# Optimization experiments

Hardware: AMD Instinct MI355X
Metric: run time of the kernel (lower is better)

The kernel has to match this reference:

```python
import jax, jax.numpy as jnp
import numpy as np


def setup_inputs() -> dict:
    key = jax.random.key(0)
    k1, k2, k3 = jax.random.split(key, 3)
    Q, M, D = 4096, 8192, 128
    query = jax.random.normal(k1, (Q, D), dtype=jnp.float32)
    memory_states = jax.random.normal(k2, (M, D), dtype=jnp.float32)
    weights = jax.random.uniform(k3, (Q, M), dtype=jnp.float32)
    return {"query": query, "memory_states": memory_states, "weights": weights}


def reference(query, memory_states, weights):
    d_k = query.shape[-1]
    # scores: [Q, M]
    scores = jnp.einsum('qd,md->qm', query, memory_states) / jnp.sqrt(jnp.asarray(d_k, query.dtype))
    attn = jax.nn.softmax(scores * weights, axis=-1)
    return jnp.einsum('qm,md->qd', attn, memory_states)
```

## Files before the change

kernel.cpp:

```cpp
#include <hip/hip_runtime.h>
#include <hip/hip_bf16.h>

typedef __attribute__((ext_vector_type(8))) short bf16x8;
typedef __attribute__((ext_vector_type(4))) float f32x4;

#define Qn 4096
#define Mn 8192
#define Dn 128
#define NWA 8
#define QB 128
#define MSPLIT 16
#define BCOLS (Mn / MSPLIT)
#define TILE 64
#define NIT (BCOLS / TILE)

__device__ __forceinline__ unsigned short f2bf(float x) {
  __hip_bfloat16 h = __float2bfloat16(x);
  return *reinterpret_cast<unsigned short*>(&h);
}

__device__ __forceinline__ void gld_lds16(const void* g, void* l) {
  __builtin_amdgcn_global_load_lds(
      (const __attribute__((address_space(1))) unsigned int*)g,
      (__attribute__((address_space(3))) unsigned int*)l, 16, 0, 0);
}

__global__ void zero_kernel(float4* __restrict__ p, int n4) {
  int i = blockIdx.x * blockDim.x + threadIdx.x;
  if (i < n4) p[i] = make_float4(0.f, 0.f, 0.f, 0.f);
}

__global__ void cast_q(const float4* __restrict__ Q4, ushort4* __restrict__ Qs) {
  int i = blockIdx.x * blockDim.x + threadIdx.x;
  const float s = 0.088388347648318447f;
  float4 q = Q4[i];
  Qs[i] = make_ushort4(f2bf(q.x * s), f2bf(q.y * s), f2bf(q.z * s), f2bf(q.w * s));
}

__global__ __launch_bounds__(256) void swz_kernel(const float* __restrict__ K,
                                                  unsigned short* __restrict__ Kswz,
                                                  unsigned short* __restrict__ Vswz) {
  __shared__ __align__(16) unsigned short T[64][72];
  const int m0 = blockIdx.x * 64, d0 = blockIdx.y * 64;
  const int t = threadIdx.x;
  const int r = t >> 4, c4 = (t & 15) * 4;
#pragma unroll
  for (int rr = 0; rr < 64; rr += 16) {
    float4 v = *reinterpret_cast<const float4*>(&K[(size_t)(m0 + r + rr) * Dn + d0 + c4]);
    ushort4 b = make_ushort4(f2bf(v.x), f2bf(v.y), f2bf(v.z), f2bf(v.w));
    *reinterpret_cast<ushort4*>(&T[r + rr][c4]) = b;
  }
  __syncthreads();
#pragma unroll
  for (int rep = 0; rep < 2; ++rep) {
    int w = t + rep * 256;
    int ml = w >> 3, oct = w & 7;
    uint4 val = *reinterpret_cast<uint4*>(&T[ml][oct * 8]);
    int m = m0 + ml, d = d0 + oct * 8;
    int g = m >> 4, l = m & 15, kk = d >> 5, quad = (d >> 3) & 3;
    *reinterpret_cast<uint4*>(&Kswz[(size_t)(((g * 4 + kk) * 64) + quad * 16 + l) * 8]) = val;
  }
#pragma unroll
  for (int rep = 0; rep < 2; ++rep) {
    int w = t + rep * 256;
    int dl = w >> 3, moct = w & 7;
    unsigned short tmp[8];
#pragma unroll
    for (int j = 0; j < 8; ++j) tmp[j] = T[moct * 8 + j][dl];
    int d = d0 + dl, m = m0 + moct * 8;
    int np = d >> 4, lB = d & 15, mt = m >> 6, mm = m & 63, kk2 = mm >> 5, qB = (mm >> 3) & 3;
    *reinterpret_cast<uint4*>(
        &Vswz[(size_t)((((mt * 8 + np) * 2 + kk2) * 64) + qB * 16 + lB) * 8]) =
        *reinterpret_cast<uint4*>(tmp);
  }
}

__global__ __launch_bounds__(512) __attribute__((amdgpu_waves_per_eu(4, 4)))
void attn_kernel(const float* __restrict__ W,
                 const unsigned short* __restrict__ Qs,
                 const unsigned short* __restrict__ Kswz,
                 const unsigned short* __restrict__ Vswz,
                 float* __restrict__ Oacc,
                 float* __restrict__ Lacc) {
  __shared__ __align__(16) unsigned short Klds[16 * 64 * 8];
  __shared__ __align__(16) unsigned short Vlds[16 * 64 * 8];
  __shared__ __align__(16) unsigned char  WP[NWA][4096];

  const int tid  = threadIdx.x;
  const int wave = tid >> 6;
  const int lane = tid & 63;
  const int l    = lane & 15;
  const int quad = lane >> 4;
  const int b    = blockIdx.x;
  const int qb   = (b >> 4) * QB;
  const int mbeg = (b & 15) * BCOLS;
  const int qw   = qb + wave * 16;

  bf16x8 aq[4];
  {
    const unsigned short* qrow = Qs + (size_t)(qw + l) * Dn + quad * 8;
#pragma unroll
    for (int kk = 0; kk < 4; ++kk)
      aq[kk] = *reinterpret_cast<const bf16x8*>(qrow + 32 * kk);
  }

  f32x4 O[8];
#pragma unroll
  for (int n = 0; n < 8; ++n) O[n] = (f32x4){0.f, 0.f, 0.f, 0.f};
  float lsum[4] = {0.f, 0.f, 0.f, 0.f};

  for (int it = 0; it < NIT; ++it) {
    const int m0 = mbeg + it * TILE;
    __syncthreads();

    {
      const unsigned short* ksrc = Kswz + (size_t)m0 * 128;
      const unsigned short* vsrc = Vswz + (size_t)m0 * 128;
#pragma unroll
      for (int i = 0; i < 2; ++i) {
        const int c = wave * 2 + i;
        gld_lds16(ksrc + (size_t)c * 512 + lane * 8, &Klds[c * 512]);
        gld_lds16(vsrc + (size_t)c * 512 + lane * 8, &Vlds[c * 512]);
      }
    }
#pragma unroll
    for (int i = 0; i < 4; ++i) {
      const float* wsrc = &W[(size_t)(qw + i * 4 + (lane >> 4)) * Mn + m0 +
                             (((lane & 15) * 4) ^ (i * 16))];
      gld_lds16(wsrc, &WP[wave][i * 1024]);
    }
    __syncthreads();

    f32x4 S[4];
#pragma unroll
    for (int a = 0; a < 4; ++a) S[a] = (f32x4){0.f, 0.f, 0.f, 0.f};
#pragma unroll
    for (int a = 0; a < 4; ++a)
#pragma unroll
      for (int kk = 0; kk < 4; ++kk) {
        bf16x8 bk = *reinterpret_cast<const bf16x8*>(
            &Klds[((a * 4 + kk) * 64 + lane) * 8]);
        S[a] = __builtin_amdgcn_mfma_f32_16x16x32_bf16(aq[kk], bk, S[a], 0, 0, 0);
      }

    float wv[16];
#pragma unroll
    for (int a = 0; a < 4; ++a)
#pragma unroll
      for (int r = 0; r < 4; ++r)
        wv[a * 4 + r] = *reinterpret_cast<const float*>(
            &WP[wave][(size_t)(((quad * 4 + r) * 64) +
                               ((16 * a + l) ^ (quad * 16))) * 4]);
    asm volatile("s_waitcnt lgkmcnt(0)" ::: "memory");

    unsigned short* P = reinterpret_cast<unsigned short*>(&WP[wave][0]);
#pragma unroll
    for (int a = 0; a < 4; ++a)
#pragma unroll
      for (int r = 0; r < 4; ++r) {
        float p = __expf(S[a][r] * wv[a * 4 + r]);
        lsum[r] += p;
        P[(quad * 4 + r) * 72 + 16 * a + l] = f2bf(p);
      }
    asm volatile("s_waitcnt lgkmcnt(0)" ::: "memory");

#pragma unroll
    for (int kk = 0; kk < 2; ++kk) {
      bf16x8 pa = *reinterpret_cast<const bf16x8*>(
          &P[l * 72 + 32 * kk + quad * 8]);
#pragma unroll
      for (int n = 0; n < 8; ++n) {
        bf16x8 bv = *reinterpret_cast<const bf16x8*>(
            &Vlds[((n * 2 + kk) * 64 + lane) * 8]);
        O[n] = __builtin_amdgcn_mfma_f32_16x16x32_bf16(pa, bv, O[n], 0, 0, 0);
      }
    }
  }

#pragma unroll
  for (int r = 0; r < 4; ++r)
#pragma unroll
    for (int off = 1; off < 16; off <<= 1)
      lsum[r] += __shfl_xor(lsum[r], off, 64);

#pragma unroll
  for (int n = 0; n < 8; ++n)
#pragma unroll
    for (int r = 0; r < 4; ++r)
      atomicAdd(&Oacc[(size_t)(qw + quad * 4 + r) * Dn + 16 * n + l], O[n][r]);
  if (l == 0)
#pragma unroll
    for (int r = 0; r < 4; ++r) atomicAdd(&Lacc[qw + quad * 4 + r], lsum[r]);
}

__global__ void finalize_kernel(const float4* __restrict__ Oacc,
                                const float* __restrict__ Lacc,
                                float4* __restrict__ out) {
  int i = blockIdx.x * blockDim.x + threadIdx.x;
  float4 o = Oacc[i];
  float inv = 1.0f / Lacc[i >> 5];
  out[i] = make_float4(o.x * inv, o.y * inv, o.z * inv, o.w * inv);
}

extern "C" void kernel_launch(void* const* d_in, const int* in_sizes, int n_in,
                              void* d_out, int out_size, void* d_ws, size_t ws_size,
                              hipStream_t stream) {
  const float* Q = (const float*)d_in[0];
  const float* K = (const float*)d_in[1];
  const float* W = (const float*)d_in[2];
  float* out = (float*)d_out;

  unsigned short* Qs   = (unsigned short*)d_ws;
  unsigned short* Kswz = Qs + (size_t)Qn * Dn;
  unsigned short* Vswz = Kswz + (size_t)Mn * Dn;
  float* Oacc = (float*)(Vswz + (size_t)Mn * Dn);
  float* Lacc = Oacc + (size_t)Qn * Dn;

  int n4 = (Qn * Dn + Qn) / 4;
  zero_kernel<<<(n4 + 255) / 256, 256, 0, stream>>>((float4*)Oacc, n4);

  cast_q<<<(Qn * Dn / 4) / 256, 256, 0, stream>>>((const float4*)Q, (ushort4*)Qs);
  swz_kernel<<<dim3(Mn / 64, Dn / 64), 256, 0, stream>>>(K, Kswz, Vswz);
  attn_kernel<<<(Qn / QB) * MSPLIT, 512, 0, stream>>>(W, Qs, Kswz, Vswz, Oacc, Lacc);
  finalize_kernel<<<(Qn * Dn / 4) / 256, 256, 0, stream>>>(
      (const float4*)Oacc, Lacc, (float4*)out);
}
```

Measured before the change: 231.0 us.

## Process two 16-row query subtiles per wave to reuse K/V LDS fragments

```diff
diff --git a/kernel.cpp b/kernel.cpp
--- a/kernel.cpp
+++ b/kernel.cpp
@@ -7,7 +7,7 @@
 #define Qn 4096
 #define Mn 8192
 #define Dn 128
-#define NWA 8
+#define NWA 4
 #define QB 128
 #define MSPLIT 16
 #define BCOLS (Mn / MSPLIT)
@@ -75,7 +75,7 @@
   }
 }
 
-__global__ __launch_bounds__(512) __attribute__((amdgpu_waves_per_eu(4, 4)))
+__global__ __launch_bounds__(256) __attribute__((amdgpu_waves_per_eu(2, 2)))
 void attn_kernel(const float* __restrict__ W,
                  const unsigned short* __restrict__ Qs,
                  const unsigned short* __restrict__ Kswz,
@@ -84,7 +84,7 @@
                  float* __restrict__ Lacc) {
   __shared__ __align__(16) unsigned short Klds[16 * 64 * 8];
   __shared__ __align__(16) unsigned short Vlds[16 * 64 * 8];
-  __shared__ __align__(16) unsigned char  WP[NWA][4096];
+  __shared__ __align__(16) unsigned char  WP[NWA][8192];
 
   const int tid  = threadIdx.x;
   const int wave = tid >> 6;
@@ -94,20 +94,23 @@
   const int b    = blockIdx.x;
   const int qb   = (b >> 4) * QB;
   const int mbeg = (b & 15) * BCOLS;
-  const int qw   = qb + wave * 16;
-
-  bf16x8 aq[4];
-  {
-    const unsigned short* qrow = Qs + (size_t)(qw + l) * Dn + quad * 8;
+  const int qw   = qb + wave * 32;
+
+  bf16x8 aq[2][4];
+#pragma unroll
+  for (int sub = 0; sub < 2; ++sub) {
+    const unsigned short* qrow = Qs + (size_t)(qw + sub * 16 + l) * Dn + quad * 8;
 #pragma unroll
     for (int kk = 0; kk < 4; ++kk)
-      aq[kk] = *reinterpret_cast<const bf16x8*>(qrow + 32 * kk);
-  }
-
-  f32x4 O[8];
-#pragma unroll
-  for (int n = 0; n < 8; ++n) O[n] = (f32x4){0.f, 0.f, 0.f, 0.f};
-  float lsum[4] = {0.f, 0.f, 0.f, 0.f};
+      aq[sub][kk] = *reinterpret_cast<const bf16x8*>(qrow + 32 * kk);
+  }
+
+  f32x4 O[2][8];
+#pragma unroll
+  for (int sub = 0; sub < 2; ++sub)
+#pragma unroll
+    for (int n = 0; n < 8; ++n) O[sub][n] = (f32x4){0.f, 0.f, 0.f, 0.f};
+  float lsum[2][4] = {{0.f, 0.f, 0.f, 0.f}, {0.f, 0.f, 0.f, 0.f}};
 
   for (int it = 0; it < NIT; ++it) {
     const int m0 = mbeg + it * TILE;
@@ -117,80 +120,97 @@
       const unsigned short* ksrc = Kswz + (size_t)m0 * 128;
       const unsigned short* vsrc = Vswz + (size_t)m0 * 128;
 #pragma unroll
-      for (int i = 0; i < 2; ++i) {
-        const int c = wave * 2 + i;
+      for (int i = 0; i < 4; ++i) {
+        const int c = wave * 4 + i;
         gld_lds16(ksrc + (size_t)c * 512 + lane * 8, &Klds[c * 512]);
         gld_lds16(vsrc + (size_t)c * 512 + lane * 8, &Vlds[c * 512]);
       }
     }
 #pragma unroll
-    for (int i = 0; i < 4; ++i) {
+    for (int i = 0; i < 8; ++i) {
       const float* wsrc = &W[(size_t)(qw + i * 4 + (lane >> 4)) * Mn + m0 +
-                             (((lane & 15) * 4) ^ (i * 16))];
+                             (((lane & 15) * 4) ^ ((i & 3) * 16))];
       gld_lds16(wsrc, &WP[wave][i * 1024]);
     }
     __syncthreads();
 
-    f32x4 S[4];
-#pragma unroll
-    for (int a = 0; a < 4; ++a) S[a] = (f32x4){0.f, 0.f, 0.f, 0.f};
+    f32x4 S[2][4];
+#pragma unroll
+    for (int sub = 0; sub < 2; ++sub)
+#pragma unroll
+      for (int a = 0; a < 4; ++a) S[sub][a] = (f32x4){0.f, 0.f, 0.f, 0.f};
 #pragma unroll
     for (int a = 0; a < 4; ++a)
 #pragma unroll
       for (int kk = 0; kk < 4; ++kk) {
         bf16x8 bk = *reinterpret_cast<const bf16x8*>(
             &Klds[((a * 4 + kk) * 64 + lane) * 8]);
-        S[a] = __builtin_amdgcn_mfma_f32_16x16x32_bf16(aq[kk], bk, S[a], 0, 0, 0);
+        S[0][a] = __builtin_amdgcn_mfma_f32_16x16x32_bf16(aq[0][kk], bk, S[0][a], 0, 0, 0);
+        S[1][a] = __builtin_amdgcn_mfma_f32_16x16x32_bf16(aq[1][kk], bk, S[1][a], 0, 0, 0);
       }
 
-    float wv[16];
-#pragma unroll
-    for (int a = 0; a < 4; ++a)
-#pragma unroll
-      for (int r = 0; r < 4; ++r)
-        wv[a * 4 + r] = *reinterpret_cast<const float*>(
-            &WP[wave][(size_t)(((quad * 4 + r) * 64) +
-                               ((16 * a + l) ^ (quad * 16))) * 4]);
+    float wv[2][16];
+#pragma unroll
+    for (int sub = 0; sub < 2; ++sub)
+#pragma unroll
+      for (int a = 0; a < 4; ++a)
+#pragma unroll
+        for (int r = 0; r < 4; ++r)
+          wv[sub][a * 4 + r] = *reinterpret_cast<const float*>(
+              &WP[wave][(size_t)(((sub * 16 + quad * 4 + r) * 64) +
+                                 ((16 * a + l) ^ (quad * 16))) * 4]);
     asm volatile("s_waitcnt lgkmcnt(0)" ::: "memory");
 
     unsigned short* P = reinterpret_cast<unsigned short*>(&WP[wave][0]);
 #pragma unroll
-    for (int a = 0; a < 4; ++a)
-#pragma unroll
-      for (int r = 0; r < 4; ++r) {
-        float p = __expf(S[a][r] * wv[a * 4 + r]);
-        lsum[r] += p;
-        P[(quad * 4 + r) * 72 + 16 * a + l] = f2bf(p);
-      }
+    for (int sub = 0; sub < 2; ++sub)
+#pragma unroll
+      for (int a = 0; a < 4; ++a)
+#pragma unroll
+        for (int r = 0; r < 4; ++r) {
+          float p = __expf(S[sub][a][r] * wv[sub][a * 4 + r]);
+          lsum[sub][r] += p;
+          P[(sub * 16 + quad * 4 + r) * 72 + 16 * a + l] = f2bf(p);
+        }
     asm volatile("s_waitcnt lgkmcnt(0)" ::: "memory");
 
 #pragma unroll
     for (int kk = 0; kk < 2; ++kk) {
-      bf16x8 pa = *reinterpret_cast<const bf16x8*>(
-          &P[l * 72 + 32 * kk + quad * 8]);
+      bf16x8 pa0 = *reinterpret_cast<const bf16x8*>(
+          &P[(0 * 16 + l) * 72 + 32 * kk + quad * 8]);
+      bf16x8 pa1 = *reinterpret_cast<const bf16x8*>(
+          &P[(1 * 16 + l) * 72 + 32 * kk + quad * 8]);
 #pragma unroll
       for (int n = 0; n < 8; ++n) {
         bf16x8 bv = *reinterpret_cast<const bf16x8*>(
             &Vlds[((n * 2 + kk) * 64 + lane) * 8]);
-        O[n] = __builtin_amdgcn_mfma_f32_16x16x32_bf16(pa, bv, O[n], 0, 0, 0);
+        O[0][n] = __builtin_amdgcn_mfma_f32_16x16x32_bf16(pa0, bv, O[0][n], 0, 0, 0);
+        O[1][n] = __builtin_amdgcn_mfma_f32_16x16x32_bf16(pa1, bv, O[1][n], 0, 0, 0);
       }
     }
   }
 
 #pragma unroll
-  for (int r = 0; r < 4; ++r)
-#pragma unroll
-    for (int off = 1; off < 16; off <<= 1)
-      lsum[r] += __shfl_xor(lsum[r], off, 64);
-
-#pragma unroll
-  for (int n = 0; n < 8; ++n)
+  for (int sub = 0; sub < 2; ++sub)
 #pragma unroll
     for (int r = 0; r < 4; ++r)
-      atomicAdd(&Oacc[(size_t)(qw + quad * 4 + r) * Dn + 16 * n + l], O[n][r]);
-  if (l == 0)
-#pragma unroll
-    for (int r = 0; r < 4; ++r) atomicAdd(&Lacc[qw + quad * 4 + r], lsum[r]);
+#pragma unroll
+      for (int off = 1; off < 16; off <<= 1)
+        lsum[sub][r] += __shfl_xor(lsum[sub][r], off, 64);
+
+#pragma unroll
+  for (int sub = 0; sub < 2; ++sub) {
+#pragma unroll
+    for (int n = 0; n < 8; ++n)
+#pragma unroll
+      for (int r = 0; r < 4; ++r)
+        atomicAdd(&Oacc[(size_t)(qw + sub * 16 + quad * 4 + r) * Dn + 16 * n + l],
+                  O[sub][n][r]);
+    if (l == 0)
+#pragma unroll
+      for (int r = 0; r < 4; ++r)
+        atomicAdd(&Lacc[qw + sub * 16 + quad * 4 + r], lsum[sub][r]);
+  }
 }
 
 __global__ void finalize_kernel(const float4* __restrict__ Oacc,
@@ -221,7 +241,7 @@
 
   cast_q<<<(Qn * Dn / 4) / 256, 256, 0, stream>>>((const float4*)Q, (ushort4*)Qs);
   swz_kernel<<<dim3(Mn / 64, Dn / 64), 256, 0, stream>>>(K, Kswz, Vswz);
-  attn_kernel<<<(Qn / QB) * MSPLIT, 512, 0, stream>>>(W, Qs, Kswz, Vswz, Oacc, Lacc);
+  attn_kernel<<<(Qn / QB) * MSPLIT, 256, 0, stream>>>(W, Qs, Kswz, Vswz, Oacc, Lacc);
   finalize_kernel<<<(Qn * Dn / 4) / 256, 256, 0, stream>>>(
       (const float4*)Oacc, Lacc, (float4*)out);
 }
```

Measured after the change: 241.1 us. 1.04x slower.
